# Optimization experiments

Hardware: AMD Instinct MI355X
Metric: run time of the kernel (lower is better)

The kernel has to match this reference:

```python
import jax, jax.numpy as jnp
import numpy as np

B, S, D, H = 2, 2048, 1024, 16
DK = D // H
THETA = 10000.0


def apply_rope(t, pos):
    # t: [B, H, S, DK], pos: [B, S] int
    half = DK // 2
    inv_freq = THETA ** (-jnp.arange(0, DK, 2, dtype=jnp.float32) / DK)  # [half]
    ang = pos.astype(jnp.float32)[:, None, :, None] * inv_freq  # [B,1,S,half]
    cos, sin = jnp.cos(ang), jnp.sin(ang)
    t1, t2 = t[..., 0::2], t[..., 1::2]  # interleaved pairs
    r1 = t1 * cos - t2 * sin
    r2 = t1 * sin + t2 * cos
    return jnp.stack([r1, r2], axis=-1).reshape(t.shape)


def setup_inputs() -> dict:
    key = jax.random.key(0)
    ks = jax.random.split(key, 5)
    x = jax.random.normal(ks[0], (B, S, D), dtype=jnp.float32)
    scale = 0.02
    Wq = jax.random.normal(ks[1], (D, D), dtype=jnp.float32) * scale
    Wk = jax.random.normal(ks[2], (D, D), dtype=jnp.float32) * scale
    Wv = jax.random.normal(ks[3], (D, D), dtype=jnp.float32) * scale
    Wo = jax.random.normal(ks[4], (D, D), dtype=jnp.float32) * scale
    token_positions = jnp.broadcast_to(jnp.arange(S, dtype=jnp.int64), (B, S))
    return {"x": x, "Wq": Wq, "Wk": Wk, "Wv": Wv, "Wo": Wo,
            "token_positions": token_positions}


def reference(x, Wq, Wk, Wv, Wo, token_positions):
    # Bias-free linear projections: y = x @ W^T (torch Linear convention)
    q = jnp.einsum('bsd,ed->bse', x, Wq)
    k = jnp.einsum('bsd,ed->bse', x, Wk)
    v = jnp.einsum('bsd,ed->bse', x, Wv)
    # split heads: [B, S, H*DK] -> [B, H, S, DK]
    def split(t):
        return t.reshape(B, S, H, DK).transpose(0, 2, 1, 3)
    qh, kh, vh = split(q), split(k), split(v)
    qh = apply_rope(qh, token_positions)
    kh = apply_rope(kh, token_positions)
    scores = jnp.einsum('bhqd,bhkd->bhqk', qh, kh) / jnp.sqrt(jnp.float32(DK))
    causal = jnp.tril(jnp.ones((S, S), dtype=bool))
    scores = jnp.where(causal, scores, jnp.finfo(scores.dtype).min)
    probs = jax.nn.softmax(scores, axis=-1)
    out = jnp.einsum('bhqk,bhkd->bhqd', probs, vh)  # [B,H,S,DK]
    out = out.transpose(0, 2, 1, 3).reshape(B, S, D)
    return jnp.einsum('bsd,ed->bse', out, Wo)
```

## Files before the change

### kernel.cpp

```cpp
#include <hip/hip_runtime.h>
#include <stdint.h>

#define B_  2
#define S_  2048
#define D_  1024
#define H_  16
#define DK_ 64

using bf16x8 = __attribute__((ext_vector_type(8))) short;
using f32x4  = __attribute__((ext_vector_type(4))) float;

__device__ __forceinline__ unsigned short f2bf(float f) {
    union { float f; uint32_t u; } v; v.f = f;
    uint32_t r = v.u + 0x7FFFu + ((v.u >> 16) & 1u);
    return (unsigned short)(r >> 16);
}

__device__ __forceinline__ uint32_t cvtpk(float lo, float hi) {
    uint32_t r;
    asm("v_cvt_pk_bf16_f32 %0, %1, %2" : "=v"(r) : "v"(lo), "v"(hi));
    return r;
}
__device__ __forceinline__ void ps32(uint32_t& a, uint32_t& b) {
    asm volatile("v_permlane32_swap_b32 %0, %1" : "+v"(a), "+v"(b));
}
__device__ __forceinline__ void ps16(uint32_t& a, uint32_t& b) {
    asm volatile("v_permlane16_swap_b32 %0, %1" : "+v"(a), "+v"(b));
}

#define GLD16(G, L) __builtin_amdgcn_global_load_lds( \
    (const __attribute__((address_space(1))) void*)(const void*)(G), \
    (__attribute__((address_space(3))) void*)(void*)(L), 16, 0, 0)

__global__ __launch_bounds__(256) void k_f32_to_bf16(const float* __restrict__ src,
                                                     unsigned short* __restrict__ dst,
                                                     int n4) {
    int i = blockIdx.x * 256 + threadIdx.x;
    if (i >= n4) return;
    float4 v = ((const float4*)src)[i];
    union { unsigned short u[4]; uint2 d; } o;
    o.u[0] = f2bf(v.x); o.u[1] = f2bf(v.y); o.u[2] = f2bf(v.z); o.u[3] = f2bf(v.w);
    ((uint2*)dst)[i] = o.d;
}

__global__ __launch_bounds__(256) void k_wconv(
    const float* __restrict__ s0, const float* __restrict__ s1,
    const float* __restrict__ s2, const float* __restrict__ s3,
    unsigned short* __restrict__ d0, unsigned short* __restrict__ d1,
    unsigned short* __restrict__ d2, unsigned short* __restrict__ d3) {
    const int w = blockIdx.y;
    const float* s = w == 0 ? s0 : w == 1 ? s1 : w == 2 ? s2 : s3;
    unsigned short* d = w == 0 ? d0 : w == 1 ? d1 : w == 2 ? d2 : d3;
    int i = blockIdx.x * 256 + threadIdx.x;
    float4 v = ((const float4*)s)[i];
    union { unsigned short u[4]; uint2 dd; } o;
    o.u[0] = f2bf(v.x); o.u[1] = f2bf(v.y); o.u[2] = f2bf(v.z); o.u[3] = f2bf(v.w);
    ((uint2*)d)[i] = o.dd;
}

template<int MODE>
__global__ __launch_bounds__(256) void k_gemm_bt(
    const unsigned short* __restrict__ A,
    const unsigned short* __restrict__ W0,
    const unsigned short* __restrict__ W1,
    const unsigned short* __restrict__ W2,
    void* __restrict__ C0, void* __restrict__ C1, void* __restrict__ C2,
    int M, int N, int K)
{
    __shared__ __align__(16) unsigned short As[2][128 * 32];
    __shared__ __align__(16) unsigned short Bs[2][128 * 32];

    const int tid  = threadIdx.x;
    const int wid  = tid >> 6, lane = tid & 63;
    const int m16  = lane & 15, g = lane >> 4;
    const int m0   = blockIdx.x * 128, n0 = blockIdx.y * 128;
    const unsigned short* Wm = blockIdx.z == 0 ? W0 : (blockIdx.z == 1 ? W1 : W2);
    void* Cm = blockIdx.z == 0 ? C0 : (blockIdx.z == 1 ? C1 : C2);

    const int wm = (wid >> 1) * 64, wn = (wid & 1) * 64;
    const int srow = lane >> 2;
    const int scol = ((lane & 3) ^ ((lane >> 3) & 3)) * 8;
    const int sw8  = (m16 >> 1) & 3;

    const f32x4 fz = {0.f, 0.f, 0.f, 0.f};
    f32x4 acc[4][4];
#pragma unroll
    for (int i = 0; i < 4; ++i)
#pragma unroll
        for (int j = 0; j < 4; ++j) acc[i][j] = fz;

#pragma unroll
    for (int c = 0; c < 2; ++c) {
        const int chunk = wid * 2 + c;
        const int row   = chunk * 16 + srow;
        GLD16(A  + (size_t)(m0 + row) * K + scol, &As[0][chunk * 512]);
        GLD16(Wm + (size_t)(n0 + row) * K + scol, &Bs[0][chunk * 512]);
    }
    __syncthreads();

    int buf = 0;
    for (int k0 = 0; k0 < K; k0 += 32) {
        if (k0 + 32 < K) {
#pragma unroll
            for (int c = 0; c < 2; ++c) {
                const int chunk = wid * 2 + c;
                const int row   = chunk * 16 + srow;
                GLD16(A  + (size_t)(m0 + row) * K + k0 + 32 + scol, &As[buf ^ 1][chunk * 512]);
                GLD16(Wm + (size_t)(n0 + row) * K + k0 + 32 + scol, &Bs[buf ^ 1][chunk * 512]);
            }
        }
        bf16x8 af[4], bf[4];
#pragma unroll
        for (int i = 0; i < 4; ++i)
            af[i] = *(const bf16x8*)(&As[buf][(wm + i * 16 + m16) * 32 + ((g ^ sw8) * 8)]);
#pragma unroll
        for (int j = 0; j < 4; ++j)
            bf[j] = *(const bf16x8*)(&Bs[buf][(wn + j * 16 + m16) * 32 + ((g ^ sw8) * 8)]);
#pragma unroll
        for (int i = 0; i < 4; ++i)
#pragma unroll
            for (int j = 0; j < 4; ++j)
                acc[i][j] = __builtin_amdgcn_mfma_f32_16x16x32_bf16(af[i], bf[j], acc[i][j], 0, 0, 0);
        __syncthreads();
        buf ^= 1;
    }

#pragma unroll
    for (int i = 0; i < 4; ++i) {
#pragma unroll
        for (int j = 0; j < 4; ++j) {
#pragma unroll
            for (int r = 0; r < 4; ++r) {
                const int row = m0 + wm + i * 16 + g * 4 + r;
                const int col = n0 + wn + j * 16 + m16;
                const float val = acc[i][j][r];
                if (MODE == 1) {
                    ((float*)Cm)[(size_t)row * N + col] = val;
                } else {
                    const int b = row >> 11, s = row & (S_ - 1);
                    const int h = col >> 6,  dk = col & (DK_ - 1);
                    size_t idx;
                    if (blockIdx.z == 2)
                        idx = ((size_t)((b * H_ + h) * DK_ + dk)) * S_ + s;
                    else
                        idx = ((size_t)((b * H_ + h) * S_ + s)) * DK_ + dk;
                    ((unsigned short*)Cm)[idx] = f2bf(val);
                }
            }
        }
    }
}

__global__ __launch_bounds__(256) void k_rope_inplace(
    unsigned short* __restrict__ qh, unsigned short* __restrict__ kh,
    const int* __restrict__ tok)
{
    const int idx = blockIdx.x * 256 + threadIdx.x;
    const int c = idx & 7;
    const int s = (idx >> 3) & (S_ - 1);
    const int b = idx >> 18;
    const size_t off = (size_t)idx * 8;

    const float pos = (float)tok[b * S_ + s];
    float cs[4], sn[4];
#pragma unroll
    for (int i = 0; i < 4; ++i) {
        const int p = c * 4 + i;
        const float inv = exp2f((float)(-2 * p) * (13.287712379549449f / 64.f));
        sincosf(pos * inv, &sn[i], &cs[i]);
    }
    bf16x8 qv = *(bf16x8*)(qh + off);
    bf16x8 kv = *(bf16x8*)(kh + off);
    bf16x8 qo, ko;
#pragma unroll
    for (int i = 0; i < 4; ++i) {
        union { uint32_t u; float f; } q1{(uint32_t)(unsigned short)qv[2*i] << 16};
        union { uint32_t u; float f; } q2{(uint32_t)(unsigned short)qv[2*i+1] << 16};
        qo[2 * i]     = (short)f2bf(q1.f * cs[i] - q2.f * sn[i]);
        qo[2 * i + 1] = (short)f2bf(q1.f * sn[i] + q2.f * cs[i]);
        union { uint32_t u; float f; } k1{(uint32_t)(unsigned short)kv[2*i] << 16};
        union { uint32_t u; float f; } k2{(uint32_t)(unsigned short)kv[2*i+1] << 16};
        ko[2 * i]     = (short)f2bf(k1.f * cs[i] - k2.f * sn[i]);
        ko[2 * i + 1] = (short)f2bf(k1.f * sn[i] + k2.f * cs[i]);
    }
    *(bf16x8*)(qh + off) = qo;
    *(bf16x8*)(kh + off) = ko;
}

__global__ __launch_bounds__(256, 2) void k_fattn6(
    const unsigned short* __restrict__ Q,
    const unsigned short* __restrict__ K,
    const unsigned short* __restrict__ Vt,
    unsigned short* __restrict__ O)
{
    __shared__ __align__(16) unsigned short Ks[2][64 * 64];
    __shared__ __align__(16) unsigned short Vs[2][64 * 64];

    const int tid = threadIdx.x, wid = tid >> 6, lane = tid & 63;
    const int m16 = lane & 15, g = lane >> 4;
    const int bh = blockIdx.x & 31;
    const int j  = blockIdx.x >> 5;
    const int b = bh >> 4, h = bh & 15;
    const unsigned short* Qb = Q  + (size_t)bh * S_ * DK_;
    const unsigned short* Kb = K  + (size_t)bh * S_ * DK_;
    const unsigned short* Vb = Vt + (size_t)bh * DK_ * S_;

    const int r8   = lane >> 3;
    const int slot = (lane & 7) ^ r8;
    const int ch0  = wid * 2, ch1 = wid * 2 + 1;

    const f32x4 fz = {0.f, 0.f, 0.f, 0.f};
    const float kSc = 0.125f * 1.4426950408889634f;

    GLD16(Kb + (size_t)(ch0 * 8 + r8) * DK_ + slot * 8, &Ks[0][ch0 * 512]);
    GLD16(Kb + (size_t)(ch1 * 8 + r8) * DK_ + slot * 8, &Ks[0][ch1 * 512]);
    GLD16(Vb + (size_t)(ch0 * 8 + r8) * S_  + slot * 8, &Vs[0][ch0 * 512]);
    GLD16(Vb + (size_t)(ch1 * 8 + r8) * S_  + slot * 8, &Vs[0][ch1 * 512]);
    __syncthreads();

    int buf = 0;
#pragma unroll
    for (int ph = 0; ph < 2; ++ph) {
        const int qi = ph ? 31 - j : j;
        const int q0 = qi * 64;
        const int qw0 = q0 + wid * 16;

        bf16x8 qf[2];
        {
            const unsigned short* qp = Qb + (size_t)(qw0 + m16) * DK_ + g * 8;
            qf[0] = *(const bf16x8*)(qp);
            qf[1] = *(const bf16x8*)(qp + 32);
        }

        f32x4 o[4];
#pragma unroll
        for (int i = 0; i < 4; ++i) o[i] = fz;
        float ps = 0.f;

        const int nt = qi + 1;
        for (int t = 0; t < nt; ++t) {
            const int kv0 = t * 64;
            int nkv0 = -1;
            if (t + 1 < nt)      nkv0 = kv0 + 64;
            else if (ph == 0)    nkv0 = 0;
            if (nkv0 >= 0) {
                GLD16(Kb + (size_t)(nkv0 + ch0 * 8 + r8) * DK_ + slot * 8, &Ks[buf ^ 1][ch0 * 512]);
                GLD16(Kb + (size_t)(nkv0 + ch1 * 8 + r8) * DK_ + slot * 8, &Ks[buf ^ 1][ch1 * 512]);
                GLD16(Vb + (size_t)(ch0 * 8 + r8) * S_ + nkv0 + slot * 8, &Vs[buf ^ 1][ch0 * 512]);
                GLD16(Vb + (size_t)(ch1 * 8 + r8) * S_ + nkv0 + slot * 8, &Vs[buf ^ 1][ch1 * 512]);
            }

            f32x4 sc[4];
            __builtin_amdgcn_s_setprio(1);
#pragma unroll
            for (int c = 0; c < 4; ++c) {
                const int row = c * 16 + m16, rr = row & 7;
                bf16x8 kf0 = *(const bf16x8*)(&Ks[buf][row * 64 + ((g ^ rr) << 3)]);
                bf16x8 kf1 = *(const bf16x8*)(&Ks[buf][row * 64 + (((4 + g) ^ rr) << 3)]);
                f32x4 z = fz;
                z = __builtin_amdgcn_mfma_f32_16x16x32_bf16(kf0, qf[0], z, 0, 0, 0);
                z = __builtin_amdgcn_mfma_f32_16x16x32_bf16(kf1, qf[1], z, 0, 0, 0);
                sc[c] = z;
            }
            __builtin_amdgcn_s_setprio(0);

            bf16x8 vf[2][4];
#pragma unroll
            for (int c2 = 0; c2 < 4; ++c2) {
                const int rv = (c2 * 16 + m16) & 7;
                vf[0][c2] = *(const bf16x8*)(&Vs[buf][(c2 * 16 + m16) * 64 + ((g ^ rv) << 3)]);
                vf[1][c2] = *(const bf16x8*)(&Vs[buf][(c2 * 16 + m16) * 64 + (((4 + g) ^ rv) << 3)]);
            }

            const bool maskT = (t == qi);
            const int qrow = qw0 + m16;
            uint32_t pk[4][2];
#pragma unroll
            for (int c = 0; c < 4; ++c) {
                float p[4];
#pragma unroll
                for (int r = 0; r < 4; ++r) {
                    float v = exp2f(sc[c][r] * kSc);
                    if (maskT && (kv0 + c * 16 + g * 4 + r > qrow)) v = 0.f;
                    p[r] = v;
                }
                ps += (p[0] + p[1]) + (p[2] + p[3]);
                pk[c][0] = cvtpk(p[0], p[1]);
                pk[c][1] = cvtpk(p[2], p[3]);
            }

            bf16x8 pf[2];
#pragma unroll
            for (int ks = 0; ks < 2; ++ks) {
                uint32_t ylo = pk[2 * ks][0], zlo = pk[2 * ks + 1][0];
                ps32(ylo, zlo); ps16(ylo, zlo);
                uint32_t yhi = pk[2 * ks][1], zhi = pk[2 * ks + 1][1];
                ps32(yhi, zhi); ps16(yhi, zhi);
                union { uint32_t u[4]; bf16x8 v; } fu;
                fu.u[0] = ylo; fu.u[1] = yhi; fu.u[2] = zlo; fu.u[3] = zhi;
                pf[ks] = fu.v;
            }

            __builtin_amdgcn_s_setprio(1);
#pragma unroll
            for (int c2 = 0; c2 < 4; ++c2) {
                o[c2] = __builtin_amdgcn_mfma_f32_16x16x32_bf16(pf[0], vf[0][c2], o[c2], 0, 0, 0);
                o[c2] = __builtin_amdgcn_mfma_f32_16x16x32_bf16(pf[1], vf[1][c2], o[c2], 0, 0, 0);
            }
            __builtin_amdgcn_s_setprio(0);

            __syncthreads();
            buf ^= 1;
        }

        float s = ps;
        s += __shfl_xor(s, 16);
        s += __shfl_xor(s, 32);
        const float inv = 1.f / s;
        float lrq[4];
#pragma unroll
        for (int r = 0; r < 4; ++r)
            lrq[r] = __shfl(inv, g * 4 + r);
#pragma unroll
        for (int c2 = 0; c2 < 4; ++c2)
#pragma unroll
            for (int r = 0; r < 4; ++r) {
                const int orow = qw0 + g * 4 + r;
                const int ocol = h * DK_ + c2 * 16 + m16;
                O[((size_t)(b * S_ + orow)) * D_ + ocol] = f2bf(o[c2][r] * lrq[r]);
            }
    }
}

extern "C" void kernel_launch(void* const* d_in, const int* in_sizes, int n_in,
                              void* d_out, int out_size, void* d_ws, size_t ws_size,
                              hipStream_t stream) {
    (void)in_sizes; (void)n_in; (void)out_size; (void)ws_size;
    const float* x   = (const float*)d_in[0];
    const float* Wq  = (const float*)d_in[1];
    const float* Wk  = (const float*)d_in[2];
    const float* Wv  = (const float*)d_in[3];
    const float* Wo  = (const float*)d_in[4];
    const int*   tok = (const int*)d_in[5];

    char* ws = (char*)d_ws;
    const size_t MB = 1u << 20;
    unsigned short* xb  = (unsigned short*)(ws + 0 * MB);
    unsigned short* wqb = (unsigned short*)(ws + 8 * MB);
    unsigned short* wkb = (unsigned short*)(ws + 10 * MB);
    unsigned short* wvb = (unsigned short*)(ws + 12 * MB);
    unsigned short* wob = (unsigned short*)(ws + 14 * MB);
    unsigned short* qh  = (unsigned short*)(ws + 16 * MB);
    unsigned short* kh  = (unsigned short*)(ws + 24 * MB);
    unsigned short* vh  = (unsigned short*)(ws + 32 * MB);
    unsigned short* ao  = (unsigned short*)(ws + 40 * MB);

    k_f32_to_bf16<<<4096, 256, 0, stream>>>(x, xb, (B_ * S_ * D_) / 4);
    k_wconv<<<dim3(1024, 4), 256, 0, stream>>>(Wq, Wk, Wv, Wo, wqb, wkb, wvb, wob);

    k_gemm_bt<0><<<dim3(32, 8, 3), 256, 0, stream>>>(
        xb, wqb, wkb, wvb, qh, kh, vh, B_ * S_, D_, D_);

    k_rope_inplace<<<2048, 256, 0, stream>>>(qh, kh, tok);

    k_fattn6<<<dim3(512), 256, 0, stream>>>(qh, kh, vh, ao);

    k_gemm_bt<1><<<dim3(32, 8, 1), 256, 0, stream>>>(
        ao, wob, wob, wob, d_out, d_out, d_out, B_ * S_, D_, D_);
}
```

Baseline: 122.6 us.

## Fuse RoPE into QKV GEMM epilogue, merge prep kernels, use MFMA row sums

The separate RoPE kernel is removed. RoPE is now applied in the QKV GEMM epilogue, using a lane-pair shuffle and a precomputed cos/sin table. The x and weight bf16 conversions and the table generation are merged into one prep launch. In attention, the softmax row sums come from an extra MFMA against a ones vector instead of scalar adds and cross-lane shuffles. This removes a full read and write of Q and K plus two launches, at the cost of a table lookup in the GEMM epilogue and two extra MFMAs per attention tile.

```diff
diff --git a/kernel.cpp b/kernel.cpp
--- a/kernel.cpp
+++ b/kernel.cpp
@@ -32,30 +32,39 @@
     (const __attribute__((address_space(1))) void*)(const void*)(G), \
     (__attribute__((address_space(3))) void*)(void*)(L), 16, 0, 0)
 
-__global__ __launch_bounds__(256) void k_f32_to_bf16(const float* __restrict__ src,
-                                                     unsigned short* __restrict__ dst,
-                                                     int n4) {
-    int i = blockIdx.x * 256 + threadIdx.x;
-    if (i >= n4) return;
-    float4 v = ((const float4*)src)[i];
-    union { unsigned short u[4]; uint2 d; } o;
-    o.u[0] = f2bf(v.x); o.u[1] = f2bf(v.y); o.u[2] = f2bf(v.z); o.u[3] = f2bf(v.w);
-    ((uint2*)dst)[i] = o.d;
-}
-
-__global__ __launch_bounds__(256) void k_wconv(
-    const float* __restrict__ s0, const float* __restrict__ s1,
-    const float* __restrict__ s2, const float* __restrict__ s3,
-    unsigned short* __restrict__ d0, unsigned short* __restrict__ d1,
-    unsigned short* __restrict__ d2, unsigned short* __restrict__ d3) {
-    const int w = blockIdx.y;
-    const float* s = w == 0 ? s0 : w == 1 ? s1 : w == 2 ? s2 : s3;
-    unsigned short* d = w == 0 ? d0 : w == 1 ? d1 : w == 2 ? d2 : d3;
-    int i = blockIdx.x * 256 + threadIdx.x;
-    float4 v = ((const float4*)s)[i];
-    union { unsigned short u[4]; uint2 dd; } o;
-    o.u[0] = f2bf(v.x); o.u[1] = f2bf(v.y); o.u[2] = f2bf(v.z); o.u[3] = f2bf(v.w);
-    ((uint2*)d)[i] = o.dd;
+__global__ __launch_bounds__(256) void k_prep(
+    const float* __restrict__ x,
+    const float* __restrict__ Wq, const float* __restrict__ Wk,
+    const float* __restrict__ Wv, const float* __restrict__ Wo,
+    unsigned short* __restrict__ xb,
+    unsigned short* __restrict__ wqb, unsigned short* __restrict__ wkb,
+    unsigned short* __restrict__ wvb, unsigned short* __restrict__ wob,
+    float2* __restrict__ trig)
+{
+    const int bid = blockIdx.x, tid = threadIdx.x;
+    if (bid < 4096) {
+        const int i = bid * 256 + tid;
+        float4 v = ((const float4*)x)[i];
+        union { unsigned short u[4]; uint2 d; } o;
+        o.u[0] = f2bf(v.x); o.u[1] = f2bf(v.y); o.u[2] = f2bf(v.z); o.u[3] = f2bf(v.w);
+        ((uint2*)xb)[i] = o.d;
+    } else if (bid < 8192) {
+        const int w = (bid - 4096) >> 10;
+        const float* s = w == 0 ? Wq : w == 1 ? Wk : w == 2 ? Wv : Wo;
+        unsigned short* d = w == 0 ? wqb : w == 1 ? wkb : w == 2 ? wvb : wob;
+        const int i = ((bid - 4096) & 1023) * 256 + tid;
+        float4 v = ((const float4*)s)[i];
+        union { unsigned short u[4]; uint2 dd; } o;
+        o.u[0] = f2bf(v.x); o.u[1] = f2bf(v.y); o.u[2] = f2bf(v.z); o.u[3] = f2bf(v.w);
+        ((uint2*)d)[i] = o.dd;
+    } else {
+        const int idx = (bid - 8192) * 256 + tid;
+        const int p = idx & 31, pos = idx >> 5;
+        const float inv = exp2f((float)(-2 * p) * (13.287712379549449f / 64.f));
+        float sn, cs;
+        sincosf((float)pos * inv, &sn, &cs);
+        trig[idx] = make_float2(cs, sn);
+    }
 }
 
 template<int MODE>
@@ -65,7 +74,8 @@
     const unsigned short* __restrict__ W1,
     const unsigned short* __restrict__ W2,
     void* __restrict__ C0, void* __restrict__ C1, void* __restrict__ C2,
-    int M, int N, int K)
+    int M, int N, int K,
+    const int* __restrict__ tok, const float2* __restrict__ trig)
 {
     __shared__ __align__(16) unsigned short As[2][128 * 32];
     __shared__ __align__(16) unsigned short Bs[2][128 * 32];
@@ -125,6 +135,7 @@
         buf ^= 1;
     }
 
+    const bool doRope = (MODE == 0) && (blockIdx.z < 2);
 #pragma unroll
     for (int i = 0; i < 4; ++i) {
 #pragma unroll
@@ -133,12 +144,19 @@
             for (int r = 0; r < 4; ++r) {
                 const int row = m0 + wm + i * 16 + g * 4 + r;
                 const int col = n0 + wn + j * 16 + m16;
-                const float val = acc[i][j][r];
+                float val = acc[i][j][r];
                 if (MODE == 1) {
                     ((float*)Cm)[(size_t)row * N + col] = val;
                 } else {
                     const int b = row >> 11, s = row & (S_ - 1);
                     const int h = col >> 6,  dk = col & (DK_ - 1);
+                    const float part = __shfl_xor(val, 1);
+                    if (doRope) {
+                        const int pos = tok[b * S_ + s];
+                        const float2 cs = trig[pos * 32 + (dk >> 1)];
+                        val = (dk & 1) ? (part * cs.y + val * cs.x)
+                                       : (val * cs.x - part * cs.y);
+                    }
                     size_t idx;
                     if (blockIdx.z == 2)
                         idx = ((size_t)((b * H_ + h) * DK_ + dk)) * S_ + s;
@@ -151,43 +169,7 @@
     }
 }
 
-__global__ __launch_bounds__(256) void k_rope_inplace(
-    unsigned short* __restrict__ qh, unsigned short* __restrict__ kh,
-    const int* __restrict__ tok)
-{
-    const int idx = blockIdx.x * 256 + threadIdx.x;
-    const int c = idx & 7;
-    const int s = (idx >> 3) & (S_ - 1);
-    const int b = idx >> 18;
-    const size_t off = (size_t)idx * 8;
-
-    const float pos = (float)tok[b * S_ + s];
-    float cs[4], sn[4];
-#pragma unroll
-    for (int i = 0; i < 4; ++i) {
-        const int p = c * 4 + i;
-        const float inv = exp2f((float)(-2 * p) * (13.287712379549449f / 64.f));
-        sincosf(pos * inv, &sn[i], &cs[i]);
-    }
-    bf16x8 qv = *(bf16x8*)(qh + off);
-    bf16x8 kv = *(bf16x8*)(kh + off);
-    bf16x8 qo, ko;
-#pragma unroll
-    for (int i = 0; i < 4; ++i) {
-        union { uint32_t u; float f; } q1{(uint32_t)(unsigned short)qv[2*i] << 16};
-        union { uint32_t u; float f; } q2{(uint32_t)(unsigned short)qv[2*i+1] << 16};
-        qo[2 * i]     = (short)f2bf(q1.f * cs[i] - q2.f * sn[i]);
-        qo[2 * i + 1] = (short)f2bf(q1.f * sn[i] + q2.f * cs[i]);
-        union { uint32_t u; float f; } k1{(uint32_t)(unsigned short)kv[2*i] << 16};
-        union { uint32_t u; float f; } k2{(uint32_t)(unsigned short)kv[2*i+1] << 16};
-        ko[2 * i]     = (short)f2bf(k1.f * cs[i] - k2.f * sn[i]);
-        ko[2 * i + 1] = (short)f2bf(k1.f * sn[i] + k2.f * cs[i]);
-    }
-    *(bf16x8*)(qh + off) = qo;
-    *(bf16x8*)(kh + off) = ko;
-}
-
-__global__ __launch_bounds__(256, 2) void k_fattn6(
+__global__ __launch_bounds__(256, 2) void k_fattn6b(
     const unsigned short* __restrict__ Q,
     const unsigned short* __restrict__ K,
     const unsigned short* __restrict__ Vt,
@@ -211,6 +193,9 @@
 
     const f32x4 fz = {0.f, 0.f, 0.f, 0.f};
     const float kSc = 0.125f * 1.4426950408889634f;
+    union { uint32_t u[4]; bf16x8 v; } one_;
+    one_.u[0] = one_.u[1] = one_.u[2] = one_.u[3] = 0x3F803F80u;
+    const bf16x8 ones = one_.v;
 
     GLD16(Kb + (size_t)(ch0 * 8 + r8) * DK_ + slot * 8, &Ks[0][ch0 * 512]);
     GLD16(Kb + (size_t)(ch1 * 8 + r8) * DK_ + slot * 8, &Ks[0][ch1 * 512]);
@@ -235,7 +220,7 @@
         f32x4 o[4];
 #pragma unroll
         for (int i = 0; i < 4; ++i) o[i] = fz;
-        float ps = 0.f;
+        f32x4 psacc = fz;
 
         const int nt = qi + 1;
         for (int t = 0; t < nt; ++t) {
@@ -284,7 +269,6 @@
                     if (maskT && (kv0 + c * 16 + g * 4 + r > qrow)) v = 0.f;
                     p[r] = v;
                 }
-                ps += (p[0] + p[1]) + (p[2] + p[3]);
                 pk[c][0] = cvtpk(p[0], p[1]);
                 pk[c][1] = cvtpk(p[2], p[3]);
             }
@@ -307,20 +291,18 @@
                 o[c2] = __builtin_amdgcn_mfma_f32_16x16x32_bf16(pf[0], vf[0][c2], o[c2], 0, 0, 0);
                 o[c2] = __builtin_amdgcn_mfma_f32_16x16x32_bf16(pf[1], vf[1][c2], o[c2], 0, 0, 0);
             }
+            psacc = __builtin_amdgcn_mfma_f32_16x16x32_bf16(pf[0], ones, psacc, 0, 0, 0);
+            psacc = __builtin_amdgcn_mfma_f32_16x16x32_bf16(pf[1], ones, psacc, 0, 0, 0);
             __builtin_amdgcn_s_setprio(0);
 
             __syncthreads();
             buf ^= 1;
         }
 
-        float s = ps;
-        s += __shfl_xor(s, 16);
-        s += __shfl_xor(s, 32);
-        const float inv = 1.f / s;
         float lrq[4];
 #pragma unroll
         for (int r = 0; r < 4; ++r)
-            lrq[r] = __shfl(inv, g * 4 + r);
+            lrq[r] = 1.f / psacc[r];
 #pragma unroll
         for (int c2 = 0; c2 < 4; ++c2)
 #pragma unroll
@@ -354,17 +336,16 @@
     unsigned short* kh  = (unsigned short*)(ws + 24 * MB);
     unsigned short* vh  = (unsigned short*)(ws + 32 * MB);
     unsigned short* ao  = (unsigned short*)(ws + 40 * MB);
-
-    k_f32_to_bf16<<<4096, 256, 0, stream>>>(x, xb, (B_ * S_ * D_) / 4);
-    k_wconv<<<dim3(1024, 4), 256, 0, stream>>>(Wq, Wk, Wv, Wo, wqb, wkb, wvb, wob);
+    float2* trig = (float2*)(ws + 40 * MB);
+
+    k_prep<<<8448, 256, 0, stream>>>(x, Wq, Wk, Wv, Wo,
+                                     xb, wqb, wkb, wvb, wob, trig);
 
     k_gemm_bt<0><<<dim3(32, 8, 3), 256, 0, stream>>>(
-        xb, wqb, wkb, wvb, qh, kh, vh, B_ * S_, D_, D_);
-
-    k_rope_inplace<<<2048, 256, 0, stream>>>(qh, kh, tok);
-
-    k_fattn6<<<dim3(512), 256, 0, stream>>>(qh, kh, vh, ao);
+        xb, wqb, wkb, wvb, qh, kh, vh, B_ * S_, D_, D_, tok, trig);
+
+    k_fattn6b<<<dim3(512), 256, 0, stream>>>(qh, kh, vh, ao);
 
     k_gemm_bt<1><<<dim3(32, 8, 1), 256, 0, stream>>>(
-        ao, wob, wob, wob, d_out, d_out, d_out, B_ * S_, D_, D_);
-}
+        ao, wob, wob, wob, d_out, d_out, d_out, B_ * S_, D_, D_, tok, trig);
+}
```

After: 129.8 us. 5.8% more time.
